# Optimization experiments

Hardware: AMD Instinct MI355X
Metric: run time of the kernel (lower is better)

## Reference

```python
import jax, jax.numpy as jnp
import numpy as np

EPS = 1e-05  # eigenvalue clamp, from module __init__ default


def setup_inputs() -> dict:
    key = jax.random.key(0)
    B, C = 8192, 64
    A = jax.random.normal(key, (B, C, C), dtype=jnp.float32)
    # Build well-conditioned SPD matrices: S = A A^T / C + 1e-3 I
    S = jnp.einsum('bij,bkj->bik', A, A) / C + 1e-3 * jnp.eye(C, dtype=jnp.float32)
    return {"S": S}


def reference(S) -> jnp.ndarray:
    """Log-Euclidean map: S = Q diag(w) Q^T -> Q diag(log(max(w, eps))) Q^T.

    Faithful to SPDLogMap.forward: compute in float32, clamp eigenvalues at eps,
    cast result back to the input dtype.
    """
    orig_dtype = S.dtype
    Sf = S.astype(jnp.float32)
    w, v = jnp.linalg.eigh(Sf)                      # w: (B, C), v: (B, C, C)
    log_w = jnp.log(jnp.maximum(w, EPS))            # clamp then log
    # Q diag(log_w) Q^T without materializing diag_embed
    result = jnp.einsum('bic,bc,bjc->bij', v, log_w, v)
    return result.astype(orig_dtype)
```

## Files before the change

### kernel.cpp

```cpp
#include <hip/hip_runtime.h>
#include <math.h>

#define NSWEEP_MAX 16
#define T2_TOL 2e-9f
#define EPS2 1e-10f


__device__ __forceinline__ float bperm_f(int idx, float x) {
    return __int_as_float(__builtin_amdgcn_ds_bpermute(idx, __float_as_int(x)));
}
__device__ __forceinline__ float rdlane_f(float x, int l) {
    return __int_as_float(__builtin_amdgcn_readlane(__float_as_int(x), l));
}

__global__ __launch_bounds__(64, 2) void spdlog_onesided(
    const float* __restrict__ S, float* __restrict__ Out, int nmat) {
    __shared__ float X[64][64];
    const int lane = threadIdx.x;
    const int b = blockIdx.x;
    if (b >= nmat) return;
    const float* Sb = S + (size_t)b * 4096;
    float* Ob = Out + (size_t)b * 4096;

    float g[64];
    #pragma unroll 64
    for (int s = 0; s < 64; ++s) g[s] = Sb[s * 64 + lane];

    float dpp = 0.0f;

    #pragma unroll 1
    for (int sweep = 0; sweep < NSWEEP_MAX; ++sweep) {
        dpp = 0.0f;
        #pragma unroll 64
        for (int s = 0; s < 64; ++s) dpp = fmaf(g[s], g[s], dpp);

        float maxt2 = 0.0f;
        #pragma unroll 1
        for (int m = 1; m < 64; ++m) {
            const int xl = lane ^ m;
            const int idx = xl << 2;
            const bool isLow = lane < xl;
            float pr[64];
            float dpq = 0.0f;
            #pragma unroll 64
            for (int s = 0; s < 64; ++s) {
                pr[s] = bperm_f(idx, g[s]);
                dpq = fmaf(g[s], pr[s], dpq);
            }
            #pragma unroll 64
            for (int s = 0; s < 64; ++s) asm("" : "+v"(pr[s]));
            const float pd = bperm_f(idx, dpp);
            const float d_lo = isLow ? dpp : pd;
            const float d_hi = isLow ? pd : dpp;
            const float t2 = dpq * dpq * __builtin_amdgcn_rcpf(dpp * pd);
            maxt2 = fmaxf(maxt2, t2);
            const float tau = (d_hi - d_lo) * __builtin_amdgcn_rcpf(2.0f * dpq);
            const float sq = __builtin_amdgcn_sqrtf(fmaf(tau, tau, 1.0f));
            float tt = __builtin_amdgcn_rcpf(fabsf(tau) + sq);
            tt = copysignf(tt, tau);
            float cc = __builtin_amdgcn_rsqf(fmaf(tt, tt, 1.0f));
            float ss = tt * cc;
            const bool tiny = fabsf(dpq) < 1e-30f;
            cc = tiny ? 1.0f : cc;
            ss = tiny ? 0.0f : ss;
            tt = tiny ? 0.0f : tt;
            const float es = isLow ? -ss : ss;
            const float t_own = isLow ? tt : -tt;
            dpp = fmaf(-t_own, dpq, dpp);
            #pragma unroll 64
            for (int s = 0; s < 64; ++s) g[s] = fmaf(cc, g[s], es * pr[s]);
        }
        maxt2 = fmaxf(maxt2, __shfl_xor(maxt2, 1));
        maxt2 = fmaxf(maxt2, __shfl_xor(maxt2, 2));
        maxt2 = fmaxf(maxt2, __shfl_xor(maxt2, 4));
        maxt2 = fmaxf(maxt2, __shfl_xor(maxt2, 8));
        maxt2 = fmaxf(maxt2, __shfl_xor(maxt2, 16));
        maxt2 = fmaxf(maxt2, __shfl_xor(maxt2, 32));
        if (maxt2 < T2_TOL) break;
    }

    float dfin = 0.0f;
    #pragma unroll 64
    for (int s = 0; s < 64; ++s) dfin = fmaf(g[s], g[s], dfin);
    const float w = 0.5f * logf(fmaxf(dfin, EPS2));
    const float rs = __builtin_amdgcn_rsqf(fmaxf(dfin, 1e-20f));

    #pragma unroll 64
    for (int s = 0; s < 64; ++s) X[s][lane] = g[s] * rs;
    __syncthreads();
    float uw[64];
    {
        const float4* rowp = (const float4*)&X[lane][0];
        #pragma unroll 16
        for (int gq = 0; gq < 16; ++gq) {
            const float4 q = rowp[gq];
            uw[4 * gq + 0] = q.x;
            uw[4 * gq + 1] = q.y;
            uw[4 * gq + 2] = q.z;
            uw[4 * gq + 3] = q.w;
        }
    }
    #pragma unroll 64
    for (int c = 0; c < 64; ++c) uw[c] *= rdlane_f(w, c);
    #pragma unroll 2
    for (int i = 0; i < 64; ++i) {
        const float4* Urow = (const float4*)&X[i][0];
        float acc = 0.0f;
        #pragma unroll 16
        for (int gq = 0; gq < 16; ++gq) {
            const float4 q = Urow[gq];
            acc = fmaf(q.x, uw[4 * gq + 0], acc);
            acc = fmaf(q.y, uw[4 * gq + 1], acc);
            acc = fmaf(q.z, uw[4 * gq + 2], acc);
            acc = fmaf(q.w, uw[4 * gq + 3], acc);
        }
        Ob[i * 64 + lane] = acc;
    }
}

extern "C" void kernel_launch(void* const* d_in, const int* in_sizes, int n_in,
                              void* d_out, int out_size, void* d_ws, size_t ws_size,
                              hipStream_t stream) {
    const float* S = (const float*)d_in[0];
    float* Out = (float*)d_out;
    const int nmat = in_sizes[0] / 4096;
    spdlog_onesided<<<nmat, 64, 0, stream>>>(S, Out, nmat);
}
```

Baseline: 4.359 ms.

## Use DPP and permlane swaps for XOR partner exchange in Jacobi sweeps

For XOR partners whose low four bits are 0, 1, 2, 3, 7 or 15, the partner column is fetched with DPP row moves plus v_permlane16/32_swap instead of ds_bpermute through the LDS crossbar. Other partners keep ds_bpermute, now written as inline asm with an explicit waitcnt. The dot-product reductions are split into four independent accumulators to shorten the FMA dependency chain. The convergence tolerance is loosened, so fewer sweeps may run, which could slightly reduce accuracy.

```diff
diff --git a/kernel.cpp b/kernel.cpp
--- a/kernel.cpp
+++ b/kernel.cpp
@@ -2,15 +2,36 @@
 #include <math.h>
 
 #define NSWEEP_MAX 16
-#define T2_TOL 2e-9f
+#define T2_TOL 1e-8f
 #define EPS2 1e-10f
 
 
-__device__ __forceinline__ float bperm_f(int idx, float x) {
-    return __int_as_float(__builtin_amdgcn_ds_bpermute(idx, __float_as_int(x)));
-}
 __device__ __forceinline__ float rdlane_f(float x, int l) {
     return __int_as_float(__builtin_amdgcn_readlane(__float_as_int(x), l));
+}
+
+#define DPP_X1 0xB1
+#define DPP_X2 0x4E
+#define DPP_X3 0x1B
+#define DPP_X7 0x141
+#define DPP_X15 0x140
+
+__device__ __forceinline__ int dpp_mov(int x, int ctrl) {
+    switch (ctrl) {
+        case DPP_X1:  return __builtin_amdgcn_update_dpp(0, x, DPP_X1, 0xF, 0xF, true);
+        case DPP_X2:  return __builtin_amdgcn_update_dpp(0, x, DPP_X2, 0xF, 0xF, true);
+        case DPP_X3:  return __builtin_amdgcn_update_dpp(0, x, DPP_X3, 0xF, 0xF, true);
+        case DPP_X7:  return __builtin_amdgcn_update_dpp(0, x, DPP_X7, 0xF, 0xF, true);
+        default:      return __builtin_amdgcn_update_dpp(0, x, DPP_X15, 0xF, 0xF, true);
+    }
+}
+__device__ __forceinline__ float swap16_self(float x) {
+    asm("v_permlane16_swap_b32 %0, %0" : "+v"(x));
+    return x;
+}
+__device__ __forceinline__ float swap32_self(float x) {
+    asm("v_permlane32_swap_b32 %0, %0" : "+v"(x));
+    return x;
 }
 
 __global__ __launch_bounds__(64, 2) void spdlog_onesided(
@@ -30,26 +51,73 @@
 
     #pragma unroll 1
     for (int sweep = 0; sweep < NSWEEP_MAX; ++sweep) {
-        dpp = 0.0f;
-        #pragma unroll 64
-        for (int s = 0; s < 64; ++s) dpp = fmaf(g[s], g[s], dpp);
+        float d0 = 0.0f, d1 = 0.0f, d2 = 0.0f, d3 = 0.0f;
+        #pragma unroll 16
+        for (int s = 0; s < 64; s += 4) {
+            d0 = fmaf(g[s], g[s], d0);
+            d1 = fmaf(g[s + 1], g[s + 1], d1);
+            d2 = fmaf(g[s + 2], g[s + 2], d2);
+            d3 = fmaf(g[s + 3], g[s + 3], d3);
+        }
+        dpp = (d0 + d1) + (d2 + d3);
 
         float maxt2 = 0.0f;
         #pragma unroll 1
         for (int m = 1; m < 64; ++m) {
             const int xl = lane ^ m;
-            const int idx = xl << 2;
             const bool isLow = lane < xl;
+            const int lo = m & 15;
+            const bool valu = (lo == 0) | (lo == 1) | (lo == 2) |
+                              (lo == 3) | (lo == 7) | (lo == 15);
             float pr[64];
-            float dpq = 0.0f;
-            #pragma unroll 64
-            for (int s = 0; s < 64; ++s) {
-                pr[s] = bperm_f(idx, g[s]);
-                dpq = fmaf(g[s], pr[s], dpq);
+            float pd;
+            if (valu) {
+                int ctrl = (lo == 1) ? DPP_X1 : (lo == 2) ? DPP_X2 :
+                           (lo == 3) ? DPP_X3 : (lo == 7) ? DPP_X7 : DPP_X15;
+                int xpd = __float_as_int(dpp);
+                if (lo) xpd = dpp_mov(xpd, ctrl);
+                if (lo) {
+                    #pragma unroll 64
+                    for (int s = 0; s < 64; ++s)
+                        pr[s] = __int_as_float(
+                            dpp_mov(__float_as_int(g[s]), ctrl));
+                } else {
+                    #pragma unroll 64
+                    for (int s = 0; s < 64; ++s) pr[s] = g[s];
+                }
+                if (m & 16) {
+                    float t = __int_as_float(xpd);
+                    xpd = __float_as_int(swap16_self(t));
+                    #pragma unroll 64
+                    for (int s = 0; s < 64; ++s) pr[s] = swap16_self(pr[s]);
+                }
+                if (m & 32) {
+                    float t = __int_as_float(xpd);
+                    xpd = __float_as_int(swap32_self(t));
+                    #pragma unroll 64
+                    for (int s = 0; s < 64; ++s) pr[s] = swap32_self(pr[s]);
+                }
+                pd = __int_as_float(xpd);
+            } else {
+                const int idx = xl << 2;
+                #pragma unroll 64
+                for (int s = 0; s < 64; ++s)
+                    asm("ds_bpermute_b32 %0, %1, %2"
+                        : "=v"(pr[s]) : "v"(idx), "v"(g[s]) : "memory");
+                asm("ds_bpermute_b32 %0, %1, %2"
+                    : "=v"(pd) : "v"(idx), "v"(dpp) : "memory");
+                asm volatile("s_waitcnt lgkmcnt(0)" ::: "memory");
+                __builtin_amdgcn_sched_barrier(0);
             }
-            #pragma unroll 64
-            for (int s = 0; s < 64; ++s) asm("" : "+v"(pr[s]));
-            const float pd = bperm_f(idx, dpp);
+            float a0 = 0.0f, a1 = 0.0f, a2 = 0.0f, a3 = 0.0f;
+            #pragma unroll 16
+            for (int s = 0; s < 64; s += 4) {
+                a0 = fmaf(g[s], pr[s], a0);
+                a1 = fmaf(g[s + 1], pr[s + 1], a1);
+                a2 = fmaf(g[s + 2], pr[s + 2], a2);
+                a3 = fmaf(g[s + 3], pr[s + 3], a3);
+            }
+            const float dpq = (a0 + a1) + (a2 + a3);
             const float d_lo = isLow ? dpp : pd;
             const float d_hi = isLow ? pd : dpp;
             const float t2 = dpq * dpq * __builtin_amdgcn_rcpf(dpp * pd);
```

Result: slower. 9.601 ms (+120.3%).
